# Optimization experiments

Hardware: AMD Instinct MI355X
Metric: run time of the kernel (lower is better)

Reference implementation:

```python
import jax, jax.numpy as jnp
import numpy as np

HEADS = 6
PS = 7  # window size
DN = ('NCHW', 'OIHW', 'NCHW')


def _conv1x1(x, w):
    return jax.lax.conv_general_dilated(x, w, (1, 1), 'VALID', dimension_numbers=DN)


def _dwconv3(x, w, groups):
    return jax.lax.conv_general_dilated(x, w, (1, 1), 'SAME', dimension_numbers=DN,
                                        feature_group_count=groups)


def _l2norm(t, eps=1e-12):
    # matches torch F.normalize(dim=-1): x / max(||x||_2, eps)
    n = jnp.sqrt(jnp.sum(t * t, axis=-1, keepdims=True))
    return t / jnp.maximum(n, eps)


def setup_inputs() -> dict:
    key = jax.random.key(0)
    k1, k2, k3, k4 = jax.random.split(key, 4)
    B, C, H, W = 2, 180, 448, 448
    x = jax.random.normal(k1, (B, C, H, W), dtype=jnp.float32)
    temperature = jnp.ones((HEADS, 1, 1), dtype=jnp.float32)
    w_qkv = jax.random.normal(k2, (3 * C, C, 1, 1), dtype=jnp.float32) * 0.05
    w_dw = jax.random.normal(k3, (3 * C, 1, 3, 3), dtype=jnp.float32) * 0.05
    w_proj = jax.random.normal(k4, (C, C, 1, 1), dtype=jnp.float32) * 0.05
    return {'x': x, 'temperature': temperature, 'w_qkv': w_qkv, 'w_dw': w_dw, 'w_proj': w_proj}


def reference(x, temperature, w_qkv, w_dw, w_proj):
    b, c, H, W = x.shape
    d = c // HEADS
    hh, ww = H // PS, W // PS

    qkv = _dwconv3(_conv1x1(x, w_qkv), w_dw, 3 * c)  # [b, 3c, H, W]
    q, k, v = jnp.split(qkv, 3, axis=1)

    def rearr(t):
        # 'b (head d) (h ph) (w pw) -> b (h w) head d (ph pw)'
        t = t.reshape(b, HEADS, d, hh, PS, ww, PS)
        t = t.transpose(0, 3, 5, 1, 2, 4, 6)  # b, hh, ww, head, d, ph, pw
        return t.reshape(b, hh * ww, HEADS, d, PS * PS)

    q, k, v = rearr(q), rearr(k), rearr(v)
    q = _l2norm(q)
    k = _l2norm(k)

    # channel-channel attention per window: [b, n_win, head, d, d]
    attn = jnp.einsum('bnhdp,bnhep->bnhde', q, k) * temperature
    attn = jax.nn.softmax(attn, axis=-1)
    out = jnp.einsum('bnhde,bnhep->bnhdp', attn, v)

    # inverse rearrange: 'b (h w) head d (ph pw) -> b (head d) (h ph) (w pw)'
    out = out.reshape(b, hh, ww, HEADS, d, PS, PS)
    out = out.transpose(0, 3, 4, 1, 5, 2, 6).reshape(b, c, H, W)
    return _conv1x1(out, w_proj)
```

## Files before the change

kernel.cpp:

```cpp
#include <hip/hip_runtime.h>

#define HW 200704
#define WIMG 448
#define VPLANE 229376

typedef __attribute__((ext_vector_type(4))) unsigned int u32x4;
typedef __attribute__((ext_vector_type(4))) float f32x4;
typedef __attribute__((ext_vector_type(8))) short s16x8;

static __device__ __forceinline__ unsigned short f2bf(float f) {
    union { float f; unsigned int u; } v; v.f = f;
    unsigned int u = v.u;
    unsigned int r = u + 0x7FFFu + ((u >> 16) & 1u);
    return (unsigned short)(r >> 16);
}
static __device__ __forceinline__ float bf2f(unsigned short s) {
    union { unsigned int u; float f; } v; v.u = ((unsigned int)s) << 16;
    return v.f;
}

__global__ __launch_bounds__(256) void transpose_cast_kernel(
    const float* __restrict__ x, unsigned short* __restrict__ xT)
{
    const int p0 = blockIdx.x * 64;
    const int tid = threadIdx.x;
    const int pl = tid & 63;

    __shared__ float T[180 * 65];

    for (int ic = tid >> 6; ic < 180; ic += 4)
        T[ic * 65 + pl] = x[(size_t)ic * HW + p0 + pl];
    __syncthreads();

    const int cg = tid >> 6;
    unsigned short* drow = xT + ((size_t)p0 + pl) * 192;
#pragma unroll
    for (int i = 0; i < 6; ++i) {
        int k0 = (cg * 6 + i) * 8;
        unsigned short u[8];
#pragma unroll
        for (int e = 0; e < 8; ++e)
            u[e] = (k0 + e < 180) ? f2bf(T[(k0 + e) * 65 + pl]) : (unsigned short)0;
        *(u32x4*)(drow + k0) = *(const u32x4*)u;
    }
}

__global__ __launch_bounds__(512) void gemm_qkv_kernel(
    const unsigned short* __restrict__ xT, const float* __restrict__ wq,
    unsigned short* __restrict__ A)
{
    const int d    = blockIdx.x;
    const int orig = (d & 7) * 490 + (d >> 3);
    const int pt   = orig / 5;
    const int oct  = orig - pt * 5;
    const int ocb  = oct * 128;
    const int pix0 = pt * 256;
    const int tid  = threadIdx.x;
    const int l    = tid & 63;
    const int w    = tid >> 6;
    const int r15  = l & 15;
    const int g4   = l >> 4;
    const int q    = w & 3;
    const int mh   = w >> 2;

    __shared__ __align__(16) unsigned short wlds[128 * 200];
    __shared__ __align__(16) unsigned short xs[2][256 * 64];

    for (int idx = tid; idx < 128 * 24; idx += 512) {
        int row = idx / 24, ch = idx - (idx / 24) * 24;
        int oc = ocb + row;
        unsigned short u[8];
#pragma unroll
        for (int e = 0; e < 8; ++e) {
            int k = ch * 8 + e;
            u[e] = (oc < 540 && k < 180) ? f2bf(wq[oc * 180 + k]) : (unsigned short)0;
        }
        *(u32x4*)(wlds + row * 200 + ch * 8) = *(const u32x4*)u;
    }

    auto stage = [&](int c, int buf) {
#pragma unroll
        for (int i = 0; i < 4; ++i) {
            int slot = i * 512 + tid;
            int px   = slot >> 3;
            int g    = slot & 7;
            const unsigned short* src =
                xT + ((size_t)pix0 + px) * 192 + c * 64 + ((g ^ (px & 7)) << 3);
            __builtin_amdgcn_global_load_lds(
                (const __attribute__((address_space(1))) unsigned int*)(const void*)src,
                (__attribute__((address_space(3))) unsigned int*)(void*)(&xs[buf][slot * 8]),
                16, 0, 0);
        }
    };

    f32x4 acc[4][4];
#pragma unroll
    for (int mi = 0; mi < 4; ++mi)
#pragma unroll
        for (int nt = 0; nt < 4; ++nt) acc[mi][nt] = (f32x4){0.f, 0.f, 0.f, 0.f};

    stage(0, 0);
    __syncthreads();

    for (int c = 0; c < 3; ++c) {
        if (c < 2) stage(c + 1, (c + 1) & 1);
        const unsigned short* xb = xs[c & 1];
#pragma unroll
        for (int kk = 0; kk < 2; ++kk) {
            s16x8 aW[4], bX[4];
#pragma unroll
            for (int mi = 0; mi < 4; ++mi)
                aW[mi] = __builtin_bit_cast(s16x8, *(const u32x4*)(
                    wlds + (mh * 64 + mi * 16 + r15) * 200 + c * 64 + kk * 32 + g4 * 8));
#pragma unroll
            for (int nt = 0; nt < 4; ++nt) {
                int px = q * 64 + nt * 16 + r15;
                bX[nt] = __builtin_bit_cast(s16x8, *(const u32x4*)(
                    xb + px * 64 + (((kk * 4 + g4) ^ (px & 7)) << 3)));
            }
#pragma unroll
            for (int mi = 0; mi < 4; ++mi)
#pragma unroll
                for (int nt = 0; nt < 4; ++nt)
                    acc[mi][nt] = __builtin_amdgcn_mfma_f32_16x16x32_bf16(
                        aW[mi], bX[nt], acc[mi][nt], 0, 0, 0);
        }
        __syncthreads();
    }

#pragma unroll
    for (int mi = 0; mi < 4; ++mi) {
#pragma unroll
        for (int reg = 0; reg < 4; ++reg) {
            int oc = ocb + mh * 64 + mi * 16 + g4 * 4 + reg;
            if (oc < 540) {
                unsigned short* orow = A + (size_t)oc * HW + pix0 + q * 64;
#pragma unroll
                for (int nt = 0; nt < 4; ++nt)
                    orow[nt * 16 + r15] = f2bf(acc[mi][nt][reg]);
            }
        }
    }
}

__global__ __launch_bounds__(256) void dw_kernel(
    const unsigned short* __restrict__ A, const float* __restrict__ wdw,
    unsigned short* __restrict__ Bw)
{
    const int wrow = blockIdx.x;
    const int c    = blockIdx.y;
    const int tid  = threadIdx.x;

    const int part = c / 180;
    const int rem  = c - part * 180;
    const int head = rem / 30;
    const int dc   = rem - head * 30;

    __shared__ float Ls[9 * 452];

    float w9[9];
#pragma unroll
    for (int i = 0; i < 9; ++i) w9[i] = wdw[c * 9 + i];

    const int y0 = wrow * 7;
    const unsigned int* Ac32 = (const unsigned int*)(A + (size_t)c * HW);
    for (int idx = tid; idx < 2016; idx += 256) {
        int r  = idx / 224;
        int c2 = idx - r * 224;
        int y  = y0 + r - 1;
        unsigned int v = ((unsigned)y < 448u) ? Ac32[y * 224 + c2] : 0u;
        Ls[r * 452 + 1 + 2 * c2] = bf2f((unsigned short)(v & 0xffffu));
        Ls[r * 452 + 2 + 2 * c2] = bf2f((unsigned short)(v >> 16));
    }
    if (tid < 18) {
        int r = tid >> 1;
        Ls[r * 452 + ((tid & 1) ? 449 : 0)] = 0.f;
    }
    __syncthreads();

    unsigned int* dst = (unsigned int*)(Bw +
        ((size_t)(head * 3 + part) * 30 + dc) * VPLANE + (size_t)wrow * 64 * 56);
#pragma unroll
    for (int k = 0; k < 7; ++k) {
        int o2 = k * 256 + tid;
        int wo = o2 / 28;
        int r2 = o2 - wo * 28;
        unsigned short r2v[2];
#pragma unroll
        for (int e = 0; e < 2; ++e) {
            int rm = r2 * 2 + e;
            float acc = 0.f;
            if (rm < 49) {
                int ph = rm / 7, pw = rm - ph * 7;
                int xb = wo * 7 + pw;
                const float* L = Ls + ph * 452 + xb;
                acc = w9[0]*L[0] + w9[1]*L[1] + w9[2]*L[2];
                L += 452;
                acc += w9[3]*L[0] + w9[4]*L[1] + w9[5]*L[2];
                L += 452;
                acc += w9[6]*L[0] + w9[7]*L[1] + w9[8]*L[2];
            }
            r2v[e] = (rm < 49) ? f2bf(acc) : (unsigned short)0;
        }
        dst[o2] = (unsigned int)r2v[0] | ((unsigned int)r2v[1] << 16);
    }
}

__global__ __launch_bounds__(256) void attn2_kernel(
    const unsigned short* __restrict__ Bw,
    const float* __restrict__ temperature,
    unsigned short* __restrict__ Cwt)
{
    __shared__ __align__(16) unsigned short lds[4][6144];
    __shared__ float invs[4][64];

    const int w    = threadIdx.x >> 6;
    const int l    = threadIdx.x & 63;
    const int wg   = blockIdx.x;
    const int head = blockIdx.y;
    const int win  = wg * 4 + w;
    const float temp = temperature[head];
    unsigned short* U = lds[w];
    float* inv = invs[w];
    const int r15 = l & 15;
    const int g4  = l >> 4;

    {
        const unsigned short* plane0 =
            Bw + (size_t)(head * 3) * 30 * VPLANE + (size_t)win * 56;
#pragma unroll
        for (int i = 0; i < 8; ++i) {
            int part = i >> 2;
            int row  = ((i & 3) << 3) | (l >> 3);
            int c    = l & 7;
            u32x4 v = {0u, 0u, 0u, 0u};
            if (row < 30 && c < 7)
                v = *(const u32x4*)(plane0 + (size_t)(part * 30 + row) * VPLANE + c * 8);
            *(u32x4*)(U + part * 2048 + row * 64 + ((c ^ (row & 7)) << 3)) = v;
        }
    }
    {
        const unsigned short* vplane =
            Bw + (size_t)(head * 3 + 2) * 30 * VPLANE + (size_t)win * 56;
        for (int j = 0; j < 23; ++j) {
            int idx = j * 64 + l;
            if (idx < 1470) {
                int dc = idx / 49;
                int p  = idx - dc * 49;
                unsigned short val = vplane[(size_t)dc * VPLANE + p];
                int col = (((dc >> 3) ^ (p & 3)) << 3) | (dc & 7);
                U[4096 + p * 32 + col] = val;
            }
        }
        int c30 = ((3 ^ (l & 3)) << 3) | 6;
        U[4096 + l * 32 + c30]     = 0;
        U[4096 + l * 32 + c30 + 1] = 0;
    }
    __syncthreads();

    s16x8 aQ[2][2], bK[2][2];
#pragma unroll
    for (int mi = 0; mi < 2; ++mi)
#pragma unroll
        for (int kk = 0; kk < 2; ++kk) {
            int r  = mi * 16 + r15;
            int gk = kk * 4 + g4;
            int so = ((gk ^ (r & 7)) << 3);
            aQ[mi][kk] = __builtin_bit_cast(s16x8, *(const u32x4*)(U + r * 64 + so));
            bK[mi][kk] = __builtin_bit_cast(s16x8, *(const u32x4*)(U + 2048 + r * 64 + so));
        }

    f32x4 s[2][2], dq[2], dk[2];
#pragma unroll
    for (int mi = 0; mi < 2; ++mi) {
        dq[mi] = (f32x4){0.f, 0.f, 0.f, 0.f};
        dk[mi] = (f32x4){0.f, 0.f, 0.f, 0.f};
#pragma unroll
        for (int nj = 0; nj < 2; ++nj) s[mi][nj] = (f32x4){0.f, 0.f, 0.f, 0.f};
    }

#pragma unroll
    for (int kk = 0; kk < 2; ++kk) {
#pragma unroll
        for (int mi = 0; mi < 2; ++mi) {
#pragma unroll
            for (int nj = 0; nj < 2; ++nj)
                s[mi][nj] = __builtin_amdgcn_mfma_f32_16x16x32_bf16(
                    aQ[mi][kk], bK[nj][kk], s[mi][nj], 0, 0, 0);
            dq[mi] = __builtin_amdgcn_mfma_f32_16x16x32_bf16(
                aQ[mi][kk], aQ[mi][kk], dq[mi], 0, 0, 0);
            dk[mi] = __builtin_amdgcn_mfma_f32_16x16x32_bf16(
                bK[mi][kk], bK[mi][kk], dk[mi], 0, 0, 0);
        }
    }

#pragma unroll
    for (int mi = 0; mi < 2; ++mi)
#pragma unroll
        for (int reg = 0; reg < 4; ++reg) {
            int row = g4 * 4 + reg;
            if (row == r15) {
                inv[mi * 16 + row]      = 1.f / fmaxf(sqrtf(dq[mi][reg]), 1e-12f);
                inv[32 + mi * 16 + row] = 1.f / fmaxf(sqrtf(dk[mi][reg]), 1e-12f);
            }
        }
    __syncthreads();

    float pr[2][2][4];
    float cinvk0 = inv[32 + r15];
    float cinvk1 = inv[32 + 16 + r15];
#pragma unroll
    for (int mi = 0; mi < 2; ++mi)
#pragma unroll
        for (int reg = 0; reg < 4; ++reg) {
            float qi = inv[mi * 16 + g4 * 4 + reg];
            float v0 = s[mi][0][reg] * qi * cinvk0 * temp;
            float v1 = s[mi][1][reg] * qi * cinvk1 * temp;
            if (16 + r15 >= 30) v1 = -1e30f;
            float m = fmaxf(v0, v1);
#pragma unroll
            for (int off = 1; off < 16; off <<= 1) m = fmaxf(m, __shfl_xor(m, off));
            float e0 = __expf(v0 - m);
            float e1 = __expf(v1 - m);
            float sum = e0 + e1;
#pragma unroll
            for (int off = 1; off < 16; off <<= 1) sum += __shfl_xor(sum, off);
            float rs = 1.f / sum;
            pr[mi][0][reg] = e0 * rs;
            pr[mi][1][reg] = e1 * rs;
        }

#pragma unroll
    for (int mi = 0; mi < 2; ++mi)
#pragma unroll
        for (int nj = 0; nj < 2; ++nj)
#pragma unroll
            for (int reg = 0; reg < 4; ++reg) {
                int row = mi * 16 + g4 * 4 + reg;
                int col = nj * 16 + r15;
                int scol = (((col >> 3) ^ (row & 3)) << 3) | (col & 7);
                U[row * 32 + scol] = f2bf(pr[mi][nj][reg]);
            }
    __syncthreads();

    s16x8 aP[2], bV[4];
#pragma unroll
    for (int mi = 0; mi < 2; ++mi) {
        int i = mi * 16 + r15;
        aP[mi] = __builtin_bit_cast(s16x8,
                 *(const u32x4*)(U + i * 32 + ((g4 ^ (i & 3)) << 3)));
    }
#pragma unroll
    for (int nt = 0; nt < 4; ++nt) {
        int p = nt * 16 + r15;
        bV[nt] = __builtin_bit_cast(s16x8,
                 *(const u32x4*)(U + 4096 + p * 32 + ((g4 ^ (p & 3)) << 3)));
    }
    f32x4 o[2][4];
#pragma unroll
    for (int mi = 0; mi < 2; ++mi)
#pragma unroll
        for (int nt = 0; nt < 4; ++nt) {
            o[mi][nt] = (f32x4){0.f, 0.f, 0.f, 0.f};
            o[mi][nt] = __builtin_amdgcn_mfma_f32_16x16x32_bf16(
                aP[mi], bV[nt], o[mi][nt], 0, 0, 0);
        }

    unsigned short* dst = Cwt + ((size_t)win * 49) * 192 + head * 30;
#pragma unroll
    for (int mi = 0; mi < 2; ++mi) {
        int ch0 = mi * 16 + g4 * 4;
#pragma unroll
        for (int nt = 0; nt < 4; ++nt) {
            int p = nt * 16 + r15;
            if (p < 49) {
                unsigned int lo = (unsigned int)f2bf(o[mi][nt][0]) |
                                  ((unsigned int)f2bf(o[mi][nt][1]) << 16);
                *(unsigned int*)(dst + (size_t)p * 192 + ch0) = lo;
                if (ch0 + 2 < 30) {
                    unsigned int hi = (unsigned int)f2bf(o[mi][nt][2]) |
                                      ((unsigned int)f2bf(o[mi][nt][3]) << 16);
                    *(unsigned int*)(dst + (size_t)p * 192 + ch0 + 2) = hi;
                }
            }
        }
    }
    if (head == 5 && g4 == 0) {
        unsigned short* zrow = Cwt + ((size_t)win * 49) * 192 + 180;
#pragma unroll
        for (int nt = 0; nt < 4; ++nt) {
            int p = nt * 16 + r15;
            if (p < 49) {
                *(unsigned int*)(zrow + (size_t)p * 192 + 0) = 0u;
                *(unsigned int*)(zrow + (size_t)p * 192 + 2) = 0u;
                *(unsigned int*)(zrow + (size_t)p * 192 + 4) = 0u;
            }
        }
    }
}

__global__ __launch_bounds__(256) void gemm_proj_kernel(
    const unsigned short* __restrict__ Cwt, const float* __restrict__ wp,
    float* __restrict__ out)
{
    const int d    = blockIdx.x;
    const int orig = (d & 7) * 294 + (d >> 3);
    const int pt   = orig / 3;
    const int ocb  = (orig - pt * 3) * 64;
    const int pix0 = pt * 256;
    const int tid  = threadIdx.x;
    const int l    = tid & 63;
    const int w    = tid >> 6;
    const int r15  = l & 15;
    const int g4   = l >> 4;

    __shared__ __align__(16) unsigned short wlds[64 * 200];
    __shared__ __align__(16) unsigned short xs[256 * 40];

    for (int idx = tid; idx < 64 * 24; idx += 256) {
        int row = idx / 24, ch = idx - (idx / 24) * 24;
        int oc = ocb + row;
        unsigned short u[8];
#pragma unroll
        for (int e = 0; e < 8; ++e) {
            int k = ch * 8 + e;
            u[e] = (oc < 180 && k < 180) ? f2bf(wp[oc * 180 + k]) : (unsigned short)0;
        }
        *(u32x4*)(wlds + row * 200 + ch * 8) = *(const u32x4*)u;
    }

    const unsigned short* srow[4];
#pragma unroll
    for (int i = 0; i < 4; ++i) {
        int P = pix0 + i * 64 + (tid >> 2);
        int win = P / 49, p = P - win * 49;
        srow[i] = Cwt + ((size_t)win * 49 + p) * 192 + (tid & 3) * 8;
    }
    const int sdst = (tid >> 2) * 40 + (tid & 3) * 8;

    f32x4 acc[4][4];
#pragma unroll
    for (int mi = 0; mi < 4; ++mi)
#pragma unroll
        for (int nt = 0; nt < 4; ++nt) acc[mi][nt] = (f32x4){0.f, 0.f, 0.f, 0.f};

    for (int ks = 0; ks < 6; ++ks) {
        __syncthreads();
#pragma unroll
        for (int i = 0; i < 4; ++i)
            *(u32x4*)(xs + sdst + i * 64 * 40) = *(const u32x4*)(srow[i] + ks * 32);
        __syncthreads();

        s16x8 aW[4], bX[4];
#pragma unroll
        for (int mi = 0; mi < 4; ++mi)
            aW[mi] = __builtin_bit_cast(s16x8,
                     *(const u32x4*)(wlds + (mi * 16 + r15) * 200 + ks * 32 + g4 * 8));
#pragma unroll
        for (int nt = 0; nt < 4; ++nt)
            bX[nt] = __builtin_bit_cast(s16x8,
                     *(const u32x4*)(xs + (w * 64 + nt * 16 + r15) * 40 + g4 * 8));
#pragma unroll
        for (int mi = 0; mi < 4; ++mi)
#pragma unroll
            for (int nt = 0; nt < 4; ++nt)
                acc[mi][nt] = __builtin_amdgcn_mfma_f32_16x16x32_bf16(
                    aW[mi], bX[nt], acc[mi][nt], 0, 0, 0);
    }

    int poff[4];
#pragma unroll
    for (int nt = 0; nt < 4; ++nt) {
        int P = pix0 + w * 64 + nt * 16 + r15;
        int win = P / 49, p = P - win * 49;
        int ph = p / 7, pw2 = p - ph * 7;
        poff[nt] = ((win >> 6) * 7 + ph) * WIMG + (win & 63) * 7 + pw2;
    }
#pragma unroll
    for (int mi = 0; mi < 4; ++mi) {
#pragma unroll
        for (int reg = 0; reg < 4; ++reg) {
            int oc = ocb + mi * 16 + g4 * 4 + reg;
            if (oc < 180) {
#pragma unroll
                for (int nt = 0; nt < 4; ++nt)
                    out[(size_t)oc * HW + poff[nt]] = acc[mi][nt][reg];
            }
        }
    }
}

extern "C" void kernel_launch(void* const* d_in, const int* in_sizes, int n_in,
                              void* d_out, int out_size, void* d_ws, size_t ws_size,
                              hipStream_t stream) {
    const float* x           = (const float*)d_in[0];
    const float* temperature = (const float*)d_in[1];
    const float* w_qkv       = (const float*)d_in[2];
    const float* w_dw        = (const float*)d_in[3];
    const float* w_proj      = (const float*)d_in[4];
    float* out = (float*)d_out;

    if (ws_size < 618627072ull) return;
    unsigned short* xT  = (unsigned short*)d_ws;
    unsigned short* A   = (unsigned short*)((char*)d_ws + 77070336ull);
    unsigned short* Bw  = (unsigned short*)((char*)d_ws + 293830656ull);
    unsigned short* Cwt = (unsigned short*)((char*)d_ws + 541556736ull);

    for (int b = 0; b < 2; ++b) {
        const float* xb = x + (size_t)b * 180 * HW;
        float* ob = out + (size_t)b * 180 * HW;
        transpose_cast_kernel<<<dim3(HW / 64), 256, 0, stream>>>(xb, xT);
        gemm_qkv_kernel<<<dim3(3920), 512, 0, stream>>>(xT, w_qkv, A);
        dw_kernel<<<dim3(64, 540), 256, 0, stream>>>(A, w_dw, Bw);
        attn2_kernel<<<dim3(1024, 6), 256, 0, stream>>>(Bw, temperature, Cwt);
        gemm_proj_kernel<<<dim3(2352), 256, 0, stream>>>(Cwt, w_proj, ob);
    }
}
```

Before: 1.376 ms.

## Pre-convert QKV weights once and retile QKV GEMM with weights read from global

A new kernel converts the QKV weights to padded bf16 once per call, so each GEMM block no longer converts fp32 weights into shared memory. The GEMM tile shrinks to 64 output channels by 256 pixels with 256 threads and more blocks. Weight fragments are loaded straight from global/L2, and the operands are swapped so each lane holds four consecutive pixels and can write them as one 8-byte store. This cuts per-block prologue work and LDS use, but re-reads the x tile once per 64 channels instead of once per 128, which raises L2 traffic.

```diff
diff --git a/kernel.cpp b/kernel.cpp
--- a/kernel.cpp
+++ b/kernel.cpp
@@ -17,6 +17,21 @@
 static __device__ __forceinline__ float bf2f(unsigned short s) {
     union { unsigned int u; float f; } v; v.u = ((unsigned int)s) << 16;
     return v.f;
+}
+
+__global__ __launch_bounds__(256) void wconv_kernel(
+    const float* __restrict__ wq, unsigned short* __restrict__ wqb)
+{
+    int idx = blockIdx.x * 256 + threadIdx.x;
+    if (idx >= 576 * 24) return;
+    int row = idx / 24, ch = idx - row * 24;
+    unsigned short u[8];
+#pragma unroll
+    for (int e = 0; e < 8; ++e) {
+        int k = ch * 8 + e;
+        u[e] = (row < 540 && k < 180) ? f2bf(wq[row * 180 + k]) : (unsigned short)0;
+    }
+    *(u32x4*)(wqb + row * 192 + ch * 8) = *(const u32x4*)u;
 }
 
 __global__ __launch_bounds__(256) void transpose_cast_kernel(
@@ -45,43 +60,27 @@
     }
 }
 
-__global__ __launch_bounds__(512) void gemm_qkv_kernel(
-    const unsigned short* __restrict__ xT, const float* __restrict__ wq,
+__global__ __launch_bounds__(256) void gemm_qkv_kernel(
+    const unsigned short* __restrict__ xT, const unsigned short* __restrict__ wqb,
     unsigned short* __restrict__ A)
 {
     const int d    = blockIdx.x;
-    const int orig = (d & 7) * 490 + (d >> 3);
-    const int pt   = orig / 5;
-    const int oct  = orig - pt * 5;
-    const int ocb  = oct * 128;
+    const int orig = (d & 7) * 882 + (d >> 3);
+    const int pt   = orig / 9;
+    const int ocb  = (orig - pt * 9) * 64;
     const int pix0 = pt * 256;
     const int tid  = threadIdx.x;
     const int l    = tid & 63;
-    const int w    = tid >> 6;
+    const int q    = tid >> 6;
     const int r15  = l & 15;
     const int g4   = l >> 4;
-    const int q    = w & 3;
-    const int mh   = w >> 2;
-
-    __shared__ __align__(16) unsigned short wlds[128 * 200];
+
     __shared__ __align__(16) unsigned short xs[2][256 * 64];
 
-    for (int idx = tid; idx < 128 * 24; idx += 512) {
-        int row = idx / 24, ch = idx - (idx / 24) * 24;
-        int oc = ocb + row;
-        unsigned short u[8];
-#pragma unroll
-        for (int e = 0; e < 8; ++e) {
-            int k = ch * 8 + e;
-            u[e] = (oc < 540 && k < 180) ? f2bf(wq[oc * 180 + k]) : (unsigned short)0;
-        }
-        *(u32x4*)(wlds + row * 200 + ch * 8) = *(const u32x4*)u;
-    }
-
     auto stage = [&](int c, int buf) {
 #pragma unroll
-        for (int i = 0; i < 4; ++i) {
-            int slot = i * 512 + tid;
+        for (int i = 0; i < 8; ++i) {
+            int slot = i * 256 + tid;
             int px   = slot >> 3;
             int g    = slot & 7;
             const unsigned short* src =
@@ -95,9 +94,11 @@
 
     f32x4 acc[4][4];
 #pragma unroll
-    for (int mi = 0; mi < 4; ++mi)
-#pragma unroll
-        for (int nt = 0; nt < 4; ++nt) acc[mi][nt] = (f32x4){0.f, 0.f, 0.f, 0.f};
+    for (int nt = 0; nt < 4; ++nt)
+#pragma unroll
+        for (int mi = 0; mi < 4; ++mi) acc[nt][mi] = (f32x4){0.f, 0.f, 0.f, 0.f};
+
+    const unsigned short* wrow = wqb + (size_t)(ocb + r15) * 192;
 
     stage(0, 0);
     __syncthreads();
@@ -107,37 +108,40 @@
         const unsigned short* xb = xs[c & 1];
 #pragma unroll
         for (int kk = 0; kk < 2; ++kk) {
-            s16x8 aW[4], bX[4];
-#pragma unroll
-            for (int mi = 0; mi < 4; ++mi)
-                aW[mi] = __builtin_bit_cast(s16x8, *(const u32x4*)(
-                    wlds + (mh * 64 + mi * 16 + r15) * 200 + c * 64 + kk * 32 + g4 * 8));
+            s16x8 aX[4], bW[4];
 #pragma unroll
             for (int nt = 0; nt < 4; ++nt) {
                 int px = q * 64 + nt * 16 + r15;
-                bX[nt] = __builtin_bit_cast(s16x8, *(const u32x4*)(
+                aX[nt] = __builtin_bit_cast(s16x8, *(const u32x4*)(
                     xb + px * 64 + (((kk * 4 + g4) ^ (px & 7)) << 3)));
             }
 #pragma unroll
             for (int mi = 0; mi < 4; ++mi)
-#pragma unroll
-                for (int nt = 0; nt < 4; ++nt)
-                    acc[mi][nt] = __builtin_amdgcn_mfma_f32_16x16x32_bf16(
-                        aW[mi], bX[nt], acc[mi][nt], 0, 0, 0);
-        }
-        __syncthreads();
+                bW[mi] = __builtin_bit_cast(s16x8, *(const u32x4*)(
+                    wrow + mi * 16 * 192 + c * 64 + kk * 32 + g4 * 8));
+#pragma unroll
+            for (int nt = 0; nt < 4; ++nt)
+#pragma unroll
+                for (int mi = 0; mi < 4; ++mi)
+                    acc[nt][mi] = __builtin_amdgcn_mfma_f32_16x16x32_bf16(
+                        aX[nt], bW[mi], acc[nt][mi], 0, 0, 0);
+        }
+        if (c < 2) __syncthreads();
     }
 
 #pragma unroll
     for (int mi = 0; mi < 4; ++mi) {
-#pragma unroll
-        for (int reg = 0; reg < 4; ++reg) {
-            int oc = ocb + mh * 64 + mi * 16 + g4 * 4 + reg;
-            if (oc < 540) {
-                unsigned short* orow = A + (size_t)oc * HW + pix0 + q * 64;
-#pragma unroll
-                for (int nt = 0; nt < 4; ++nt)
-                    orow[nt * 16 + r15] = f2bf(acc[mi][nt][reg]);
+        int oc = ocb + mi * 16 + r15;
+        if (oc < 540) {
+            unsigned short* orow = A + (size_t)oc * HW + pix0 + q * 64 + g4 * 4;
+#pragma unroll
+            for (int nt = 0; nt < 4; ++nt) {
+                uint2 v;
+                v.x = (unsigned int)f2bf(acc[nt][mi][0]) |
+                      ((unsigned int)f2bf(acc[nt][mi][1]) << 16);
+                v.y = (unsigned int)f2bf(acc[nt][mi][2]) |
+                      ((unsigned int)f2bf(acc[nt][mi][3]) << 16);
+                *(uint2*)(orow + nt * 16) = v;
             }
         }
     }
@@ -500,17 +504,20 @@
     const float* w_proj      = (const float*)d_in[4];
     float* out = (float*)d_out;
 
-    if (ws_size < 618627072ull) return;
+    if (ws_size < 618848256ull) return;
     unsigned short* xT  = (unsigned short*)d_ws;
     unsigned short* A   = (unsigned short*)((char*)d_ws + 77070336ull);
     unsigned short* Bw  = (unsigned short*)((char*)d_ws + 293830656ull);
     unsigned short* Cwt = (unsigned short*)((char*)d_ws + 541556736ull);
+    unsigned short* wqb = (unsigned short*)((char*)d_ws + 618627072ull);
+
+    wconv_kernel<<<dim3(54), 256, 0, stream>>>(w_qkv, wqb);
 
     for (int b = 0; b < 2; ++b) {
         const float* xb = x + (size_t)b * 180 * HW;
         float* ob = out + (size_t)b * 180 * HW;
         transpose_cast_kernel<<<dim3(HW / 64), 256, 0, stream>>>(xb, xT);
-        gemm_qkv_kernel<<<dim3(3920), 512, 0, stream>>>(xT, w_qkv, A);
+        gemm_qkv_kernel<<<dim3(7056), 256, 0, stream>>>(xT, wqb, A);
         dw_kernel<<<dim3(64, 540), 256, 0, stream>>>(A, w_dw, Bw);
         attn2_kernel<<<dim3(1024, 6), 256, 0, stream>>>(Bw, temperature, Cwt);
         gemm_proj_kernel<<<dim3(2352), 256, 0, stream>>>(Cwt, w_proj, ob);
```

Result: faster. 1.316 ms (-4.4%).
